# Kernel tuning notes

Measured on AMD Instinct MI355X. Metric: run time of the kernel, lower is better.

Reference implementation:

```python
import jax, jax.numpy as jnp
import numpy as np

N_NODES = 50000
N_EDGES = 1600000
F_IN = 256
OUT = 64
HEADS = 8


def setup_inputs() -> dict:
    key = jax.random.key(0)
    ks = jax.random.split(key, 6)
    x = jax.random.normal(ks[0], (N_NODES, F_IN), dtype=jnp.float32)
    edge_row = jax.random.randint(ks[1], (N_EDGES,), 0, N_NODES, dtype=jnp.int32)
    edge_col = jax.random.randint(ks[2], (N_EDGES,), 0, N_NODES, dtype=jnp.int32)
    Ws = jax.random.normal(ks[3], (HEADS, OUT, F_IN), dtype=jnp.float32) * (1.0 / np.sqrt(F_IN))
    Ws_bias = jnp.zeros((HEADS, OUT), dtype=jnp.float32)
    As = jax.random.normal(ks[4], (HEADS, 2 * OUT, 1), dtype=jnp.float32) * (1.0 / np.sqrt(OUT))
    As_bias = jnp.zeros((HEADS, 2), dtype=jnp.float32)
    return {"x": x, "edge_row": edge_row, "edge_col": edge_col,
            "Ws": Ws, "Ws_bias": Ws_bias, "As": As, "As_bias": As_bias}


def reference(x, edge_row, edge_col, Ws, Ws_bias, As, As_bias):
    # GAT forward, inference mode (training=False -> dropout rates 0).
    # Graph is a binary symmetric adjacency given as an edge list; the original's
    # sparse add of row_partial + transpose(col_partial) reduces to per-edge
    # score(i,j) = Al[i] + b0 + Ar[j] + b1 for every edge (i,j).
    # NOTE: the original computes leaky_relu(E) but then softmaxes E (lrelu is
    # discarded); we faithfully reproduce that: softmax over raw scores.
    H, O, F = Ws.shape
    N = x.shape[0]
    t = jnp.einsum('nf,hof->hno', x, Ws)                      # [H,N,O] transformed nodes
    Al = jnp.einsum('hno,ho->hn', t, As[:, :O, 0]) + As_bias[:, 0:1]  # [H,N]
    Ar = jnp.einsum('hno,ho->hn', t, As[:, O:, 0]) + As_bias[:, 1:2]  # [H,N]
    scores = Al[:, edge_row] + Ar[:, edge_col]                 # [H,E]
    seg_max = jax.vmap(lambda s: jax.ops.segment_max(s, edge_row, num_segments=N))(scores)
    seg_max = jnp.where(jnp.isfinite(seg_max), seg_max, jnp.float32(0.0))
    ex = jnp.exp(scores - seg_max[:, edge_row])                # [H,E]
    denom = jax.vmap(lambda e: jax.ops.segment_sum(e, edge_row, num_segments=N))(ex)
    alpha = ex / denom[:, edge_row]                            # row-wise sparse softmax
    # per-head aggregation (loop over small fixed head count bounds memory)
    h = jnp.stack([
        jax.ops.segment_sum(alpha[k][:, None] * t[k, edge_col, :], edge_row, num_segments=N)
        for k in range(H)
    ])                                                         # [H,N,O]
    h = h + Ws_bias[:, None, :]
    out = jnp.transpose(h, (1, 0, 2)).reshape(N, H * O)        # concat heads (reduction=False)
    return jax.nn.elu(out)
```

## Files before the change

kernel.cpp:

```cpp
#include <hip/hip_runtime.h>
#include <hip/hip_fp16.h>

#define HEADS 8
#define F_IN 256
#define OUT 64
#define NOUT 512
#define CAP 1024

#define RPB 128
#define MAXB 512
#define CHA 8192

typedef __attribute__((ext_vector_type(8))) _Float16 f16x8;
typedef __attribute__((ext_vector_type(2))) _Float16 f16x2;
typedef __attribute__((ext_vector_type(4))) float f32x4;

__device__ __forceinline__ short f2h(float f) {
  _Float16 h = (_Float16)f;
  return *(short*)&h;
}
__device__ __forceinline__ f16x2 u2h2(unsigned u) {
  union { unsigned u; f16x2 h; } x; x.u = u; return x.h;
}
__device__ __forceinline__ float h2f(unsigned short b) {
  _Float16 h = *(_Float16*)&b; return (float)h;
}

__global__ __launch_bounds__(256) void conv_kernel(
    const float* __restrict__ src, short* __restrict__ dst, int n8)
{
  int i = blockIdx.x * 256 + threadIdx.x;
  if (i >= n8) return;
  const float4 a = *(const float4*)(src + (size_t)i * 8);
  const float4 b = *(const float4*)(src + (size_t)i * 8 + 4);
  short r[8] = { f2h(a.x), f2h(a.y), f2h(a.z), f2h(a.w),
                 f2h(b.x), f2h(b.y), f2h(b.z), f2h(b.w) };
  *(uint4*)(dst + (size_t)i * 8) = *(uint4*)r;
}

__global__ __launch_bounds__(256) void va_kernel(
    const short* __restrict__ W2, const float* __restrict__ As,
    unsigned short* __restrict__ va16)
{
  const int h = blockIdx.x, k = threadIdx.x;
  const unsigned short* W = (const unsigned short*)W2;
  float s = 0.f;
  #pragma unroll 8
  for (int o = 0; o < OUT; ++o)
    s += h2f(W[(size_t)(h * OUT + o) * F_IN + k]) * As[h * 2 * OUT + OUT + o];
  va16[h * F_IN + k] = (unsigned short)f2h(s);
}

__global__ __launch_bounds__(256) void argemv_kernel(
    const short* __restrict__ xh, const unsigned short* __restrict__ va16,
    const float* __restrict__ Asb, float* __restrict__ Wf, int N)
{
  __shared__ unsigned vas[8][132];
  for (int i = threadIdx.x; i < 1024; i += 256)
    vas[i >> 7][i & 127] = ((const unsigned*)va16)[i];
  __syncthreads();
  const int t = blockIdx.x * 256 + threadIdx.x;
  const int n = t >> 3, h = t & 7;
  if (n >= N) return;
  const unsigned short* xr = (const unsigned short*)xh + (size_t)n * F_IN;
  float acc = 0.f;
  #pragma unroll
  for (int kk = 0; kk < F_IN; kk += 8) {
    const uint4 xv = *(const uint4*)(xr + kk);
    const int p2 = kk >> 1;
    acc = __builtin_amdgcn_fdot2(u2h2(xv.x), u2h2(vas[h][p2]),     acc, false);
    acc = __builtin_amdgcn_fdot2(u2h2(xv.y), u2h2(vas[h][p2 + 1]), acc, false);
    acc = __builtin_amdgcn_fdot2(u2h2(xv.z), u2h2(vas[h][p2 + 2]), acc, false);
    acc = __builtin_amdgcn_fdot2(u2h2(xv.w), u2h2(vas[h][p2 + 3]), acc, false);
  }
  Wf[t] = __expf(acc + Asb[h * 2 + 1]);
}

__global__ __launch_bounds__(256) void gemm_mfma(
    const short* __restrict__ xh, const short* __restrict__ W2,
    const float* __restrict__ Wf, short* __restrict__ u, int N)
{
  __shared__ __align__(16) short as[128][72];
  __shared__ __align__(16) short bs[64][72];
  const int ytiles = (N + 127) / 128;
  const int YB = (ytiles + 7) / 8;
  const int bid = blockIdx.x;
  const int xcd = bid & 7;
  const int j   = bid >> 3;
  const int h   = j & 7;
  const int yt  = xcd * YB + (j >> 3);
  if (yt >= ytiles) return;
  const int n0 = yt * 128;
  const int tid = threadIdx.x;
  const int lane = tid & 63, wave = tid >> 6;
  const int lcol = lane & 15, quad = lane >> 4;
  const int m0 = wave * 32;
  const short* Wh = W2 + h * OUT * F_IN;

  f32x4 acc[2][4] = {};

  for (int k0 = 0; k0 < F_IN; k0 += 64) {
    __syncthreads();
    #pragma unroll
    for (int p = 0; p < 4; ++p) {
      int id = tid + 256 * p;
      int r = id >> 3, s = id & 7;
      int n = n0 + r;
      uint4 v = make_uint4(0, 0, 0, 0);
      if (n < N) v = *(const uint4*)(xh + (size_t)n * F_IN + k0 + s * 8);
      *(uint4*)&as[r][s * 8] = v;
    }
    #pragma unroll
    for (int p = 0; p < 2; ++p) {
      int id = tid + 256 * p;
      int r = id >> 3, s = id & 7;
      uint4 v = *(const uint4*)(Wh + r * F_IN + k0 + s * 8);
      *(uint4*)&bs[r][s * 8] = v;
    }
    __syncthreads();
    #pragma unroll
    for (int ks = 0; ks < 2; ++ks) {
      f16x8 af[2], bf[4];
      #pragma unroll
      for (int i = 0; i < 2; ++i)
        af[i] = *(const f16x8*)&as[m0 + i * 16 + lcol][ks * 32 + quad * 8];
      #pragma unroll
      for (int jj = 0; jj < 4; ++jj)
        bf[jj] = *(const f16x8*)&bs[jj * 16 + lcol][ks * 32 + quad * 8];
      #pragma unroll
      for (int i = 0; i < 2; ++i)
        #pragma unroll
        for (int jj = 0; jj < 4; ++jj)
          acc[i][jj] = __builtin_amdgcn_mfma_f32_16x16x32_f16(
              af[i], bf[jj], acc[i][jj], 0, 0, 0);
    }
  }

  #pragma unroll
  for (int i = 0; i < 2; ++i) {
    #pragma unroll
    for (int reg = 0; reg < 4; ++reg) {
      int n = n0 + m0 + i * 16 + quad * 4 + reg;
      if (n < N) {
        const float w = Wf[(size_t)n * 8 + h];
        #pragma unroll
        for (int jj = 0; jj < 4; ++jj) {
          const int hp = h * 2 + (jj >> 1);
          u[((size_t)hp * N + n) * 32 + (jj & 1) * 16 + lcol] =
              f2h(acc[i][jj][reg] * w);
        }
      }
    }
  }
}

__global__ __launch_bounds__(256) void bcount_kernel(
    const int* __restrict__ row, int* __restrict__ bcnt, int E)
{
  __shared__ int h[MAXB];
  for (int i = threadIdx.x; i < MAXB; i += 256) h[i] = 0;
  __syncthreads();
  for (int e = blockIdx.x * 256 + threadIdx.x; e < E; e += gridDim.x * 256)
    atomicAdd(&h[row[e] >> 7], 1);
  __syncthreads();
  for (int i = threadIdx.x; i < MAXB; i += 256) {
    int v = h[i];
    if (v) atomicAdd(&bcnt[i], v);
  }
}

__global__ __launch_bounds__(MAXB) void bscan_kernel(
    const int* __restrict__ bcnt, int* __restrict__ bofs,
    int* __restrict__ gcur, int* __restrict__ rowptr_last, int E, int NB)
{
  __shared__ int sd[MAXB];
  const int t = threadIdx.x;
  int v = (t < NB) ? bcnt[t] : 0;
  sd[t] = v;
  __syncthreads();
  for (int off = 1; off < MAXB; off <<= 1) {
    int u = (t >= off) ? sd[t - off] : 0;
    __syncthreads();
    sd[t] += u;
    __syncthreads();
  }
  int excl = sd[t] - v;
  if (t < NB) { bofs[t] = excl; gcur[t] = excl; }
  if (t == NB - 1) bofs[NB] = excl + v;
  if (t == 0) rowptr_last[0] = E;
}

__global__ __launch_bounds__(256) void bscatter_kernel(
    const int* __restrict__ row, const int* __restrict__ col,
    int* __restrict__ gcur, unsigned* __restrict__ packed, int E)
{
  __shared__ int h[MAXB];
  __shared__ int base[MAXB];
  const int lo = blockIdx.x * CHA;
  const int hi = min(lo + CHA, E);
  for (int i = threadIdx.x; i < MAXB; i += 256) h[i] = 0;
  __syncthreads();
  for (int e = lo + threadIdx.x; e < hi; e += 256)
    atomicAdd(&h[row[e] >> 7], 1);
  __syncthreads();
  for (int i = threadIdx.x; i < MAXB; i += 256) {
    int v = h[i];
    base[i] = v ? atomicAdd(&gcur[i], v) : 0;
    h[i] = 0;
  }
  __syncthreads();
  for (int e = lo + threadIdx.x; e < hi; e += 256) {
    int r = row[e];
    int b = r >> 7;
    int p = base[b] + atomicAdd(&h[b], 1);
    packed[p] = ((unsigned)(r & (RPB - 1)) << 16) | (unsigned)col[e];
  }
}

__global__ __launch_bounds__(256) void bsort_kernel(
    const unsigned* __restrict__ packed, const int* __restrict__ bofs,
    int* __restrict__ row_ptr, int* __restrict__ col_sorted, int N)
{
  __shared__ int h[RPB];
  __shared__ int sd[RPB];
  __shared__ int cur[RPB];
  const int b = blockIdx.x;
  const int lo = bofs[b], hi = bofs[b + 1];
  const int t = threadIdx.x;
  if (t < RPB) h[t] = 0;
  __syncthreads();
  for (int i = lo + t; i < hi; i += 256)
    atomicAdd(&h[packed[i] >> 16], 1);
  __syncthreads();
  if (t < RPB) sd[t] = h[t];
  __syncthreads();
  for (int off = 1; off < RPB; off <<= 1) {
    int u = (t >= off && t < RPB) ? sd[t - off] : 0;
    __syncthreads();
    if (t < RPB) sd[t] += u;
    __syncthreads();
  }
  if (t < RPB) {
    int excl = sd[t] - h[t];
    cur[t] = lo + excl;
    int r = b * RPB + t;
    if (r < N) row_ptr[r] = lo + excl;
  }
  __syncthreads();
  for (int i = lo + t; i < hi; i += 256) {
    unsigned u = packed[i];
    int p = atomicAdd(&cur[u >> 16], 1);
    col_sorted[p] = (int)(u & 0xffffu);
  }
}

__global__ __launch_bounds__(256) void sw_kernel(
    const int* __restrict__ row_ptr, const int* __restrict__ col_sorted,
    const float* __restrict__ Wf, float* __restrict__ swb, int N)
{
  const int lane = threadIdx.x & 63;
  const int wave = threadIdx.x >> 6;
  const int row = blockIdx.x * 4 + wave;
  if (row >= N) return;
  const int start = row_ptr[row], end = row_ptr[row + 1];
  float a[8];
  #pragma unroll
  for (int i = 0; i < 8; ++i) a[i] = 0.f;
  for (int e = start + lane; e < end; e += 64) {
    int c = col_sorted[e];
    const float4 v0 = *(const float4*)(Wf + (size_t)c * 8);
    const float4 v1 = *(const float4*)(Wf + (size_t)c * 8 + 4);
    a[0] += v0.x; a[1] += v0.y; a[2] += v0.z; a[3] += v0.w;
    a[4] += v1.x; a[5] += v1.y; a[6] += v1.z; a[7] += v1.w;
  }
  #pragma unroll
  for (int off = 1; off <= 32; off <<= 1) {
    #pragma unroll
    for (int i = 0; i < 8; ++i) a[i] += __shfl_xor(a[i], off);
  }
  if (lane == 0) {
    float* sp = swb + (size_t)row * 8;
    *(float4*)sp       = make_float4(a[0], a[1], a[2], a[3]);
    *((float4*)sp + 1) = make_float4(a[4], a[5], a[6], a[7]);
  }
}

__global__ __launch_bounds__(256) void agg_kernel(
    const int* __restrict__ row_ptr, const int* __restrict__ col_sorted,
    const unsigned short* __restrict__ u, const float* __restrict__ swb,
    const float* __restrict__ Wb, float* __restrict__ out, int N, int p)
{
  __shared__ int ec[4][CAP];
  const int lane = threadIdx.x & 63;
  const int wave = threadIdx.x >> 6;
  const int head = blockIdx.x & 7;
  const int g = lane >> 2, sub = lane & 3;
  const int rbase = ((blockIdx.x >> 3) * 4 + wave) * 16;
  const int row = rbase + g;
  const bool valid = row < N;

  const int wstart = row_ptr[min(rbase, N)];
  const int wend   = row_ptr[min(rbase + 16, N)];
  const int wlen = wend - wstart;
  const int nst = min(wlen, CAP);
  int* lds = ec[wave];
  for (int i = lane; i < nst; i += 64)
    lds[i] = __builtin_nontemporal_load(col_sorted + wstart + i);
  __syncthreads();

  const int sg = valid ? row_ptr[row]     : 0;
  const int eg = valid ? row_ptr[row + 1] : 0;
  const int deg = eg - sg;
  const unsigned short* ub = u + ((size_t)(head * 2 + p) * N) * 32 + (sub << 3);

  float acc[8];
  #pragma unroll
  for (int i = 0; i < 8; ++i) acc[i] = 0.f;
  const f16x2 ones = {(_Float16)1.0f, (_Float16)1.0f};

  if (wlen <= CAP) {
    const int lsg = sg - wstart;
    const int llast = lsg + deg - 1;
    const int np = (deg + 1) >> 1;

    auto loadP = [&](int jj, int& c1, int& c2) {
      const int b = lsg + 2 * jj;
      c1 = lds[min(b, llast)];
      c2 = lds[min(b + 1, llast)];
    };
    auto issueP = [&](int c1, int c2, uint4& v1, uint4& v2) {
      v1 = *(const uint4*)(ub + (size_t)c1 * 32);
      v2 = *(const uint4*)(ub + (size_t)c2 * 32);
    };
    auto consume = [&](int jj, const uint4& v1, const uint4& v2) {
      const unsigned ma = (2 * jj     < deg) ? 0xffffffffu : 0u;
      const unsigned mb = (2 * jj + 1 < deg) ? 0xffffffffu : 0u;
      unsigned a1[4] = { v1.x & ma, v1.y & ma, v1.z & ma, v1.w & ma };
      unsigned a2[4] = { v2.x & mb, v2.y & mb, v2.z & mb, v2.w & mb };
      #pragma unroll
      for (int q = 0; q < 4; ++q) {
        unsigned plo = __builtin_amdgcn_perm(a2[q], a1[q], 0x05040100u);
        unsigned phi = __builtin_amdgcn_perm(a2[q], a1[q], 0x07060302u);
        acc[2 * q]     = __builtin_amdgcn_fdot2(u2h2(plo), ones, acc[2 * q],     false);
        acc[2 * q + 1] = __builtin_amdgcn_fdot2(u2h2(phi), ones, acc[2 * q + 1], false);
      }
    };

    if (np > 0) {
      const int nit2 = (np + 1) & ~1;
      int cA1, cA2, cB1, cB2;
      uint4 vA1, vA2, vB1, vB2;
      loadP(0, cA1, cA2); issueP(cA1, cA2, vA1, vA2);
      loadP(1, cB1, cB2); issueP(cB1, cB2, vB1, vB2);
      int j = 0;
      for (; j + 2 < nit2; j += 2) {
        consume(j, vA1, vA2);
        loadP(j + 2, cA1, cA2); issueP(cA1, cA2, vA1, vA2);
        consume(j + 1, vB1, vB2);
        loadP(j + 3, cB1, cB2); issueP(cB1, cB2, vB1, vB2);
      }
      consume(j, vA1, vA2);
      consume(j + 1, vB1, vB2);
    }
  } else {
    const int np = (deg + 1) >> 1;
    for (int j = 0; j < np; ++j) {
      const int e1 = sg + 2 * j, e2 = e1 + 1;
      const int i2 = min(e2, eg - 1);
      const int l1 = e1 - wstart, l2 = i2 - wstart;
      const int c1 = (l1 < nst) ? lds[l1]
                                : __builtin_nontemporal_load(col_sorted + e1);
      const int c2 = (l2 < nst) ? lds[l2]
                                : __builtin_nontemporal_load(col_sorted + i2);
      const uint4 v1 = *(const uint4*)(ub + (size_t)c1 * 32);
      const uint4 v2 = *(const uint4*)(ub + (size_t)c2 * 32);
      const unsigned mb = (e2 < eg) ? 0xffffffffu : 0u;
      unsigned a1[4] = { v1.x, v1.y, v1.z, v1.w };
      unsigned a2[4] = { v2.x & mb, v2.y & mb, v2.z & mb, v2.w & mb };
      #pragma unroll
      for (int q = 0; q < 4; ++q) {
        unsigned plo = __builtin_amdgcn_perm(a2[q], a1[q], 0x05040100u);
        unsigned phi = __builtin_amdgcn_perm(a2[q], a1[q], 0x07060302u);
        acc[2 * q]     = __builtin_amdgcn_fdot2(u2h2(plo), ones, acc[2 * q],     false);
        acc[2 * q + 1] = __builtin_amdgcn_fdot2(u2h2(phi), ones, acc[2 * q + 1], false);
      }
    }
  }

  if (valid) {
    const float sw = swb[(size_t)row * 8 + head];
    const float inv = (sw > 0.f) ? 1.f / sw : 0.f;
    const int bidx = head * OUT + p * 32 + (sub << 3);
    const float4 b0 = *(const float4*)(Wb + bidx);
    const float4 b1 = *(const float4*)(Wb + bidx + 4);
    const float bb[8] = { b0.x, b0.y, b0.z, b0.w, b1.x, b1.y, b1.z, b1.w };
    float r[8];
    #pragma unroll
    for (int i = 0; i < 8; ++i) {
      float y = acc[i] * inv + bb[i];
      r[i] = (y > 0.f) ? y : (__expf(y) - 1.f);
    }
    f32x4* op = (f32x4*)(out + (size_t)row * NOUT + bidx);
    f32x4 o0 = { r[0], r[1], r[2], r[3] };
    f32x4 o1 = { r[4], r[5], r[6], r[7] };
    __builtin_nontemporal_store(o0, op);
    __builtin_nontemporal_store(o1, op + 1);
  }
}

extern "C" void kernel_launch(void* const* d_in, const int* in_sizes, int n_in,
                              void* d_out, int out_size, void* d_ws, size_t ws_size,
                              hipStream_t stream)
{
  const float* x    = (const float*)d_in[0];
  const int*   erow = (const int*)d_in[1];
  const int*   ecol = (const int*)d_in[2];
  const float* Ws   = (const float*)d_in[3];
  const float* Wb   = (const float*)d_in[4];
  const float* As   = (const float*)d_in[5];
  const float* Asb  = (const float*)d_in[6];
  float* out = (float*)d_out;
  const int N = in_sizes[0] / F_IN;
  const int E = in_sizes[1];

  char* p = (char*)d_ws;
  short* u       = (short*)p; p += (size_t)HEADS * N * OUT * sizeof(short);
  short* xh      = (short*)p; p += (size_t)N * F_IN * sizeof(short);
  short* W2      = (short*)p; p += (size_t)NOUT * F_IN * sizeof(short);
  unsigned short* va16 = (unsigned short*)p; p += (size_t)HEADS * F_IN * sizeof(short);
  float* Wf      = (float*)p; p += (size_t)N * HEADS * sizeof(float);
  float* swb     = (float*)p; p += (size_t)N * HEADS * sizeof(float);
  int* row_ptr   = (int*)p;   p += (size_t)(N + 1) * sizeof(int);
  int* bcnt      = (int*)p;   p += MAXB * sizeof(int);
  int* bofs      = (int*)p;   p += (MAXB + 1) * sizeof(int);
  int* gcur      = (int*)p;   p += MAXB * sizeof(int);
  int* col_sorted= (int*)p;   p += (size_t)E * sizeof(int);
  unsigned* packed = (unsigned*)u;

  const int NB = (N + RPB - 1) / RPB;

  (void)hipMemsetAsync(bcnt, 0, MAXB * sizeof(int), stream);

  bcount_kernel<<<dim3(512), dim3(256), 0, stream>>>(erow, bcnt, E);
  bscan_kernel<<<dim3(1), dim3(MAXB), 0, stream>>>(
      bcnt, bofs, gcur, row_ptr + N, E, NB);
  bscatter_kernel<<<dim3((E + CHA - 1) / CHA), dim3(256), 0, stream>>>(
      erow, ecol, gcur, packed, E);
  bsort_kernel<<<dim3(NB), dim3(256), 0, stream>>>(
      packed, bofs, row_ptr, col_sorted, N);

  conv_kernel<<<dim3((N * F_IN / 8 + 255) / 256), dim3(256), 0, stream>>>(
      x, xh, N * F_IN / 8);
  conv_kernel<<<dim3((NOUT * F_IN / 8 + 255) / 256), dim3(256), 0, stream>>>(
      Ws, W2, NOUT * F_IN / 8);

  va_kernel<<<dim3(HEADS), dim3(F_IN), 0, stream>>>(W2, As, va16);
  argemv_kernel<<<dim3((N * HEADS + 255) / 256), dim3(256), 0, stream>>>(
      xh, va16, Asb, Wf, N);

  const int ytiles = (N + 127) / 128;
  const int YB = (ytiles + 7) / 8;
  gemm_mfma<<<dim3(8 * 8 * YB), dim3(256), 0, stream>>>(xh, W2, Wf, u, N);

  sw_kernel<<<dim3((N + 3) / 4), dim3(256), 0, stream>>>(
      row_ptr, col_sorted, Wf, swb, N);

  const int nblk = 8 * ((N + 63) / 64);
  agg_kernel<<<dim3(nblk), dim3(256), 0, stream>>>(
      row_ptr, col_sorted, (const unsigned short*)u, swb, Wb, out, N, 0);
  agg_kernel<<<dim3(nblk), dim3(256), 0, stream>>>(
      row_ptr, col_sorted, (const unsigned short*)u, swb, Wb, out, N, 1);
}
```

Measured before the change: 505.4 us.

## Add zero sentinel row and deepen aggregation gather to four edges per stage

Pads each head-half slice of the transformed feature buffer with an extra all-zero row at index N, written by a small new kernel. Out-of-range edge slots then gather that row, so the per-edge masking ANDs go away. The aggregation loop now issues four gathers per stage instead of two, double-buffered, which puts more loads in flight per lane. The cost is more registers, which may lower occupancy, plus extra padded LDS reads and wasted gathers for low-degree rows.

```diff
diff --git a/kernel.cpp b/kernel.cpp
--- a/kernel.cpp
+++ b/kernel.cpp
@@ -6,6 +6,7 @@
 #define OUT 64
 #define NOUT 512
 #define CAP 1024
+#define CAPP (CAP + 16)
 
 #define RPB 128
 #define MAXB 512
@@ -91,6 +92,7 @@
   const int yt  = xcd * YB + (j >> 3);
   if (yt >= ytiles) return;
   const int n0 = yt * 128;
+  const int NP1 = N + 1;
   const int tid = threadIdx.x;
   const int lane = tid & 63, wave = tid >> 6;
   const int lcol = lane & 15, quad = lane >> 4;
@@ -146,12 +148,19 @@
         #pragma unroll
         for (int jj = 0; jj < 4; ++jj) {
           const int hp = h * 2 + (jj >> 1);
-          u[((size_t)hp * N + n) * 32 + (jj & 1) * 16 + lcol] =
+          u[((size_t)hp * NP1 + n) * 32 + (jj & 1) * 16 + lcol] =
               f2h(acc[i][jj][reg] * w);
         }
       }
     }
   }
+}
+
+__global__ __launch_bounds__(64) void zdum_kernel(short* __restrict__ u, int N)
+{
+  const int t = threadIdx.x;
+  const int hp = t >> 2, q = t & 3;
+  *(uint4*)(u + ((size_t)hp * (N + 1) + N) * 32 + q * 8) = make_uint4(0, 0, 0, 0);
 }
 
 __global__ __launch_bounds__(256) void bcount_kernel(
@@ -290,7 +299,7 @@
     const unsigned short* __restrict__ u, const float* __restrict__ swb,
     const float* __restrict__ Wb, float* __restrict__ out, int N, int p)
 {
-  __shared__ int ec[4][CAP];
+  __shared__ int ec[4][CAPP];
   const int lane = threadIdx.x & 63;
   const int wave = threadIdx.x >> 6;
   const int head = blockIdx.x & 7;
@@ -298,6 +307,7 @@
   const int rbase = ((blockIdx.x >> 3) * 4 + wave) * 16;
   const int row = rbase + g;
   const bool valid = row < N;
+  const int NP1 = N + 1;
 
   const int wstart = row_ptr[min(rbase, N)];
   const int wend   = row_ptr[min(rbase + 16, N)];
@@ -311,7 +321,8 @@
   const int sg = valid ? row_ptr[row]     : 0;
   const int eg = valid ? row_ptr[row + 1] : 0;
   const int deg = eg - sg;
-  const unsigned short* ub = u + ((size_t)(head * 2 + p) * N) * 32 + (sub << 3);
+  const unsigned short* ub =
+      u + ((size_t)(head * 2 + p) * NP1) * 32 + (sub << 3);
 
   float acc[8];
   #pragma unroll
@@ -319,64 +330,61 @@
   const f16x2 ones = {(_Float16)1.0f, (_Float16)1.0f};
 
   if (wlen <= CAP) {
-    const int lsg = sg - wstart;
-    const int llast = lsg + deg - 1;
-    const int np = (deg + 1) >> 1;
-
-    auto loadP = [&](int jj, int& c1, int& c2) {
-      const int b = lsg + 2 * jj;
-      c1 = lds[min(b, llast)];
-      c2 = lds[min(b + 1, llast)];
-    };
-    auto issueP = [&](int c1, int c2, uint4& v1, uint4& v2) {
-      v1 = *(const uint4*)(ub + (size_t)c1 * 32);
-      v2 = *(const uint4*)(ub + (size_t)c2 * 32);
-    };
-    auto consume = [&](int jj, const uint4& v1, const uint4& v2) {
-      const unsigned ma = (2 * jj     < deg) ? 0xffffffffu : 0u;
-      const unsigned mb = (2 * jj + 1 < deg) ? 0xffffffffu : 0u;
-      unsigned a1[4] = { v1.x & ma, v1.y & ma, v1.z & ma, v1.w & ma };
-      unsigned a2[4] = { v2.x & mb, v2.y & mb, v2.z & mb, v2.w & mb };
-      #pragma unroll
-      for (int q = 0; q < 4; ++q) {
-        unsigned plo = __builtin_amdgcn_perm(a2[q], a1[q], 0x05040100u);
-        unsigned phi = __builtin_amdgcn_perm(a2[q], a1[q], 0x07060302u);
-        acc[2 * q]     = __builtin_amdgcn_fdot2(u2h2(plo), ones, acc[2 * q],     false);
-        acc[2 * q + 1] = __builtin_amdgcn_fdot2(u2h2(phi), ones, acc[2 * q + 1], false);
+    const int lsg = valid ? sg - wstart : 0;
+    const int nstg = (deg + 3) >> 2;
+    const int nstg2 = max(2, (nstg + 1) & ~1);
+
+    auto loadQ = [&](int s, int* c) {
+      const int b = lsg + 4 * s;
+      #pragma unroll
+      for (int k = 0; k < 4; ++k) {
+        int v = lds[b + k];
+        c[k] = (4 * s + k < deg) ? v : N;
       }
     };
-
-    if (np > 0) {
-      const int nit2 = (np + 1) & ~1;
-      int cA1, cA2, cB1, cB2;
-      uint4 vA1, vA2, vB1, vB2;
-      loadP(0, cA1, cA2); issueP(cA1, cA2, vA1, vA2);
-      loadP(1, cB1, cB2); issueP(cB1, cB2, vB1, vB2);
-      int j = 0;
-      for (; j + 2 < nit2; j += 2) {
-        consume(j, vA1, vA2);
-        loadP(j + 2, cA1, cA2); issueP(cA1, cA2, vA1, vA2);
-        consume(j + 1, vB1, vB2);
-        loadP(j + 3, cB1, cB2); issueP(cB1, cB2, vB1, vB2);
+    auto issueQ = [&](const int* c, uint4* v) {
+      #pragma unroll
+      for (int k = 0; k < 4; ++k)
+        v[k] = *(const uint4*)(ub + (size_t)c[k] * 32);
+    };
+    auto consumeQ = [&](const uint4* v) {
+      #pragma unroll
+      for (int pp = 0; pp < 2; ++pp) {
+        unsigned a1[4] = { v[2*pp].x, v[2*pp].y, v[2*pp].z, v[2*pp].w };
+        unsigned a2[4] = { v[2*pp+1].x, v[2*pp+1].y, v[2*pp+1].z, v[2*pp+1].w };
+        #pragma unroll
+        for (int q = 0; q < 4; ++q) {
+          unsigned plo = __builtin_amdgcn_perm(a2[q], a1[q], 0x05040100u);
+          unsigned phi = __builtin_amdgcn_perm(a2[q], a1[q], 0x07060302u);
+          acc[2 * q]     = __builtin_amdgcn_fdot2(u2h2(plo), ones, acc[2 * q],     false);
+          acc[2 * q + 1] = __builtin_amdgcn_fdot2(u2h2(phi), ones, acc[2 * q + 1], false);
+        }
       }
-      consume(j, vA1, vA2);
-      consume(j + 1, vB1, vB2);
-    }
+    };
+
+    int cA[4], cB[4];
+    uint4 vA[4], vB[4];
+    loadQ(0, cA); issueQ(cA, vA);
+    loadQ(1, cB); issueQ(cB, vB);
+    int s = 0;
+    for (; s + 2 < nstg2; s += 2) {
+      consumeQ(vA);
+      loadQ(s + 2, cA); issueQ(cA, vA);
+      consumeQ(vB);
+      loadQ(s + 3, cB); issueQ(cB, vB);
+    }
+    consumeQ(vA);
+    consumeQ(vB);
   } else {
     const int np = (deg + 1) >> 1;
     for (int j = 0; j < np; ++j) {
       const int e1 = sg + 2 * j, e2 = e1 + 1;
-      const int i2 = min(e2, eg - 1);
-      const int l1 = e1 - wstart, l2 = i2 - wstart;
-      const int c1 = (l1 < nst) ? lds[l1]
-                                : __builtin_nontemporal_load(col_sorted + e1);
-      const int c2 = (l2 < nst) ? lds[l2]
-                                : __builtin_nontemporal_load(col_sorted + i2);
+      const int c1 = (e1 < eg) ? __builtin_nontemporal_load(col_sorted + e1) : N;
+      const int c2 = (e2 < eg) ? __builtin_nontemporal_load(col_sorted + e2) : N;
       const uint4 v1 = *(const uint4*)(ub + (size_t)c1 * 32);
       const uint4 v2 = *(const uint4*)(ub + (size_t)c2 * 32);
-      const unsigned mb = (e2 < eg) ? 0xffffffffu : 0u;
       unsigned a1[4] = { v1.x, v1.y, v1.z, v1.w };
-      unsigned a2[4] = { v2.x & mb, v2.y & mb, v2.z & mb, v2.w & mb };
+      unsigned a2[4] = { v2.x, v2.y, v2.z, v2.w };
       #pragma unroll
       for (int q = 0; q < 4; ++q) {
         unsigned plo = __builtin_amdgcn_perm(a2[q], a1[q], 0x05040100u);
@@ -424,7 +432,7 @@
   const int E = in_sizes[1];
 
   char* p = (char*)d_ws;
-  short* u       = (short*)p; p += (size_t)HEADS * N * OUT * sizeof(short);
+  short* u       = (short*)p; p += (size_t)16 * (N + 1) * 32 * sizeof(short);
   short* xh      = (short*)p; p += (size_t)N * F_IN * sizeof(short);
   short* W2      = (short*)p; p += (size_t)NOUT * F_IN * sizeof(short);
   unsigned short* va16 = (unsigned short*)p; p += (size_t)HEADS * F_IN * sizeof(short);
@@ -448,6 +456,7 @@
       erow, ecol, gcur, packed, E);
   bsort_kernel<<<dim3(NB), dim3(256), 0, stream>>>(
       packed, bofs, row_ptr, col_sorted, N);
+  zdum_kernel<<<dim3(1), dim3(64), 0, stream>>>(u, N);
 
   conv_kernel<<<dim3((N * F_IN / 8 + 255) / 256), dim3(256), 0, stream>>>(
       x, xh, N * F_IN / 8);
```

Result: slower. 522.4 us (+3.4%).
